# Kernel optimization log

Hardware: AMD Instinct MI355X
Metric: run time of the kernel (lower is better)

Reference implementation:

```python
import jax, jax.numpy as jnp
import numpy as np

N_EMBED = 256
HEAD_SIZE = 64
B, T = 32, 768

def setup_inputs() -> dict:
    key = jax.random.key(0)
    kx, kq, kk, kv = jax.random.split(key, 4)
    bound = 1.0 / np.sqrt(N_EMBED)  # torch nn.Linear default init
    return {
        "x": jax.random.normal(kx, (B, T, N_EMBED), dtype=jnp.float32),
        "wq": jax.random.uniform(kq, (N_EMBED, HEAD_SIZE), minval=-bound, maxval=bound, dtype=jnp.float32),
        "wk": jax.random.uniform(kk, (N_EMBED, HEAD_SIZE), minval=-bound, maxval=bound, dtype=jnp.float32),
        "wv": jax.random.uniform(kv, (N_EMBED, HEAD_SIZE), minval=-bound, maxval=bound, dtype=jnp.float32),
    }

def reference(x, wq, wk, wv):
    # x: [B, T, C]; wq/wk/wv: [C, H]
    q = jnp.einsum('btc,ch->bth', x, wq)
    k = jnp.einsum('btc,ch->bth', x, wk)
    v = jnp.einsum('btc,ch->bth', x, wv)
    scale = k.shape[-1] ** -0.5
    scores = jnp.einsum('bqh,bkh->bqk', q, k) * scale  # [B, T, T]
    Tn = x.shape[1]
    causal = jnp.tril(jnp.ones((Tn, Tn), dtype=bool))
    scores = jnp.where(causal, scores, -jnp.inf)
    attn = jax.nn.softmax(scores, axis=-1)
    # dropout omitted (eval mode) for deterministic reference
    return jnp.einsum('bqk,bkh->bqh', attn, v)
```

## Files before the change

kernel.cpp:

```cpp
#include <hip/hip_runtime.h>
#include <hip/hip_bf16.h>

#define B_  32
#define T_  768
#define C_  256
#define H_  64
#define BT_ (B_*T_)
#define WT_OFF (3*BT_*H_)

using short8 = __attribute__((ext_vector_type(8))) short;
using f32x4  = __attribute__((ext_vector_type(4))) float;

__device__ __forceinline__ ushort f2bf(float f) {
    union { float f; unsigned u; } v; v.f = f;
    unsigned u = v.u;
    return (ushort)((u + 0x7FFFu + ((u >> 16) & 1u)) >> 16);
}

__global__ __launch_bounds__(256) void prep_w_kernel(
    const float* __restrict__ wq, const float* __restrict__ wk,
    const float* __restrict__ wv, ushort* __restrict__ ws)
{
    const int idx = blockIdx.x*256 + threadIdx.x;
    const int m = idx >> 14, r = idx & 16383;
    const int h = r >> 8, k = r & 255;
    const float* w = (m == 0) ? wq : (m == 1) ? wk : wv;
    ws[WT_OFF + idx] = f2bf(w[k*H_ + h]);
}

__global__ __launch_bounds__(256) void qkv_proj_kernel(
    const float* __restrict__ x, ushort* __restrict__ ws)
{
    __shared__ ushort wT[64][264];
    __shared__ ushort vls[64][72];
    const int tid   = threadIdx.x;
    const int wv_id = tid >> 6;
    const int lane  = tid & 63;
    const int g     = lane >> 4;
    const int c     = lane & 15;
    const int rowbase = blockIdx.x*64;
    const int row     = rowbase + wv_id*16 + c;
    const int sh = tid >> 2, ss = tid & 3;

    short8 a[8];
    const float* xr = x + row*C_;
    #pragma unroll
    for (int ch = 0; ch < 8; ++ch) {
        const float4 f0 = *(const float4*)(xr + ch*32 + g*8);
        const float4 f1 = *(const float4*)(xr + ch*32 + g*8 + 4);
        short8 t;
        t[0]=(short)f2bf(f0.x); t[1]=(short)f2bf(f0.y); t[2]=(short)f2bf(f0.z); t[3]=(short)f2bf(f0.w);
        t[4]=(short)f2bf(f1.x); t[5]=(short)f2bf(f1.y); t[6]=(short)f2bf(f1.z); t[7]=(short)f2bf(f1.w);
        a[ch] = t;
    }

    const ushort* wtg = ws + WT_OFF;
    #pragma unroll
    for (int i = 0; i < 8; ++i)
        *(short8*)&wT[sh][ss*64 + i*8] = *(const short8*)(wtg + sh*256 + ss*64 + i*8);
    __syncthreads();

    for (int m = 0; m < 3; ++m) {
        #pragma unroll
        for (int jn = 0; jn < 4; ++jn) {
            f32x4 acc = {0.f, 0.f, 0.f, 0.f};
            #pragma unroll
            for (int ch = 0; ch < 8; ++ch) {
                const short8 bw = *(const short8*)(&wT[jn*16 + c][ch*32 + g*8]);
                acc = __builtin_amdgcn_mfma_f32_16x16x32_bf16(a[ch], bw, acc, 0, 0, 0);
            }
            if (m == 0) {
                #pragma unroll
                for (int r = 0; r < 4; ++r)
                    vls[wv_id*16 + g*4 + r][jn*16 + c] = f2bf(acc[r] * 0.125f);
            } else if (m == 1) {
                #pragma unroll
                for (int r = 0; r < 4; ++r)
                    vls[wv_id*16 + g*4 + r][jn*16 + c] = f2bf(acc[r]);
            } else {
                #pragma unroll
                for (int r = 0; r < 4; ++r)
                    vls[jn*16 + c][wv_id*16 + g*4 + r] = f2bf(acc[r]);
            }
        }
        __syncthreads();
        {
            ushort* dst = (m < 2)
                ? (ws + m*BT_*H_ + (rowbase + sh)*H_ + ss*16)
                : (ws + 2*BT_*H_ + sh*BT_ + rowbase + ss*16);
            *(short8*)(dst)     = *(const short8*)&vls[sh][ss*16];
            *(short8*)(dst + 8) = *(const short8*)&vls[sh][ss*16 + 8];
            if (m < 2) {
                const ushort* src = wtg + (m+1)*16384 + sh*256 + ss*64;
                #pragma unroll
                for (int i = 0; i < 8; ++i)
                    *(short8*)&wT[sh][ss*64 + i*8] = *(const short8*)(src + i*8);
            }
        }
        __syncthreads();
    }
}

__global__ __launch_bounds__(256) void attn_kernel(
    const ushort* __restrict__ ws, float* __restrict__ out)
{
    __shared__ ushort kls[2][64][72];
    __shared__ ushort vls[2][64][72];
    __shared__ ushort pls[4][16][72];

    const int tid   = threadIdx.x;
    const int wv_id = tid >> 6;
    const int lane  = tid & 63;
    const int g     = lane >> 4;
    const int c     = lane & 15;
    const int qt    = 11 - (blockIdx.x >> 5);
    const int b     = blockIdx.x & 31;
    const int nkt   = qt + 1;
    const int sh = tid >> 2, ss = tid & 3;

    const ushort* kg  = ws + BT_*H_ + b*T_*H_;
    const ushort* vtg = ws + 2*BT_*H_ + b*T_;

    short8 aq[2];
    const ushort* qp = ws + (b*T_ + qt*64 + wv_id*16 + c)*H_;
    aq[0] = *(const short8*)(qp + g*8);
    aq[1] = *(const short8*)(qp + 32 + g*8);

    float m_ = -INFINITY, l_ = 0.f;
    f32x4 o[4];
    #pragma unroll
    for (int jh = 0; jh < 4; ++jh) o[jh] = (f32x4){0.f, 0.f, 0.f, 0.f};

    short8 kreg0, kreg1, vreg0, vreg1;
    #define LOAD_TILES(kt_) do { \
        const ushort* ksrc = kg + ((kt_)*64 + sh)*H_ + ss*16;       \
        kreg0 = *(const short8*)ksrc; kreg1 = *(const short8*)(ksrc + 8); \
        const ushort* vsrc = vtg + sh*BT_ + (kt_)*64 + ss*16;       \
        vreg0 = *(const short8*)vsrc; vreg1 = *(const short8*)(vsrc + 8); \
    } while (0)
    #define WRITE_TILES(bi_) do { \
        *(short8*)&kls[bi_][sh][ss*16]     = kreg0; \
        *(short8*)&kls[bi_][sh][ss*16 + 8] = kreg1; \
        *(short8*)&vls[bi_][sh][ss*16]     = vreg0; \
        *(short8*)&vls[bi_][sh][ss*16 + 8] = vreg1; \
    } while (0)

    LOAD_TILES(0);
    WRITE_TILES(0);
    __syncthreads();

    int cur = 0;
    for (int kt = 0; kt < nkt; ++kt) {
        const bool more = (kt + 1 < nkt);
        if (more) LOAD_TILES(kt + 1);

        f32x4 s[4];
        #pragma unroll
        for (int j = 0; j < 4; ++j) {
            f32x4 acc = {0.f, 0.f, 0.f, 0.f};
            #pragma unroll
            for (int ch = 0; ch < 2; ++ch) {
                const short8 bk = *(const short8*)(&kls[cur][j*16 + c][ch*32 + g*8]);
                acc = __builtin_amdgcn_mfma_f32_16x16x32_bf16(bk, aq[ch], acc, 0, 0, 0);
            }
            s[j] = acc;
        }

        if (kt == qt) {
            const int qloc = wv_id*16 + c;
            #pragma unroll
            for (int j = 0; j < 4; ++j)
                #pragma unroll
                for (int r = 0; r < 4; ++r)
                    if (j*16 + g*4 + r > qloc) s[j][r] = -1e30f;
        }

        float tm = s[0][0];
        #pragma unroll
        for (int j = 0; j < 4; ++j)
            #pragma unroll
            for (int r = 0; r < 4; ++r) tm = fmaxf(tm, s[j][r]);
        tm = fmaxf(tm, __shfl_xor(tm, 16));
        tm = fmaxf(tm, __shfl_xor(tm, 32));
        const float mn = fmaxf(m_, tm);
        const float al = __expf(m_ - mn);
        m_ = mn;
        float ps = 0.f;
        #pragma unroll
        for (int j = 0; j < 4; ++j)
            #pragma unroll
            for (int r = 0; r < 4; ++r) {
                const float p = __expf(s[j][r] - mn);
                s[j][r] = p;
                ps += p;
            }
        ps += __shfl_xor(ps, 16);
        ps += __shfl_xor(ps, 32);
        l_ = l_*al + ps;

        #pragma unroll
        for (int r = 0; r < 4; ++r) {
            const float alr = __shfl(al, g*4 + r);
            #pragma unroll
            for (int jh = 0; jh < 4; ++jh) o[jh][r] *= alr;
        }

        #pragma unroll
        for (int j = 0; j < 4; ++j) {
            const uint lo = (uint)f2bf(s[j][0]) | ((uint)f2bf(s[j][1]) << 16);
            const uint hi = (uint)f2bf(s[j][2]) | ((uint)f2bf(s[j][3]) << 16);
            *(uint2*)&pls[wv_id][c][j*16 + g*4] = make_uint2(lo, hi);
        }

        #pragma unroll
        for (int c2 = 0; c2 < 2; ++c2) {
            const short8 ap = *(const short8*)(&pls[wv_id][c][c2*32 + g*8]);
            #pragma unroll
            for (int jh = 0; jh < 4; ++jh) {
                const short8 bv = *(const short8*)(&vls[cur][jh*16 + c][c2*32 + g*8]);
                o[jh] = __builtin_amdgcn_mfma_f32_16x16x32_bf16(ap, bv, o[jh], 0, 0, 0);
            }
        }

        if (more) WRITE_TILES(cur ^ 1);
        __syncthreads();
        cur ^= 1;
    }

    float* op = out + (b*T_ + qt*64 + wv_id*16)*H_;
    #pragma unroll
    for (int r = 0; r < 4; ++r) {
        const float lr  = __shfl(l_, g*4 + r);
        const float inv = 1.0f / lr;
        #pragma unroll
        for (int jh = 0; jh < 4; ++jh)
            op[(g*4 + r)*H_ + jh*16 + c] = o[jh][r] * inv;
    }
    #undef LOAD_TILES
    #undef WRITE_TILES
}

extern "C" void kernel_launch(void* const* d_in, const int* in_sizes, int n_in,
                              void* d_out, int out_size, void* d_ws, size_t ws_size,
                              hipStream_t stream) {
    const float* x  = (const float*)d_in[0];
    const float* wq = (const float*)d_in[1];
    const float* wk = (const float*)d_in[2];
    const float* wv = (const float*)d_in[3];
    ushort* ws = (ushort*)d_ws;

    prep_w_kernel<<<dim3(192), dim3(256), 0, stream>>>(wq, wk, wv, ws);
    qkv_proj_kernel<<<dim3(BT_/64), dim3(256), 0, stream>>>(x, ws);
    attn_kernel<<<dim3(B_*12), dim3(256), 0, stream>>>(ws, (float*)d_out);
}
```

Measured before the change: 103.8 us.

## Fuse weight prep, QKV projection and attention into one cooperative kernel

Replaces the three kernel launches (weight transpose/convert, QKV projection, attention) with a single cooperative kernel. Each block projects the 64 rows it will later attend over, keeps Q in LDS and registers instead of writing it to global memory, and stages fp32 weights directly into LDS as bf16. K and V^T are still written to the workspace and a grid-wide sync separates projection from attention. Query tiles are paired short/long per batch to balance causal work. This removes launch gaps and the Q round trip, but adds a grid barrier, redundant per-block weight conversion, and requires all 384 blocks to be co-resident.

```diff
diff --git a/kernel.cpp b/kernel.cpp
--- a/kernel.cpp
+++ b/kernel.cpp
@@ -1,12 +1,13 @@
 #include <hip/hip_runtime.h>
 #include <hip/hip_bf16.h>
+#include <hip/hip_cooperative_groups.h>
 
 #define B_  32
 #define T_  768
 #define C_  256
 #define H_  64
 #define BT_ (B_*T_)
-#define WT_OFF (3*BT_*H_)
+#define VT_OFF (BT_*H_)
 
 using short8 = __attribute__((ext_vector_type(8))) short;
 using f32x4  = __attribute__((ext_vector_type(4))) float;
@@ -17,114 +18,103 @@
     return (ushort)((u + 0x7FFFu + ((u >> 16) & 1u)) >> 16);
 }
 
-__global__ __launch_bounds__(256) void prep_w_kernel(
-    const float* __restrict__ wq, const float* __restrict__ wk,
-    const float* __restrict__ wv, ushort* __restrict__ ws)
+__device__ __forceinline__ void stage_w(const float* __restrict__ wsrc,
+                                        ushort (*wT)[264], int tid) {
+    #pragma unroll
+    for (int j = 0; j < 16; ++j) {
+        const int base = tid*4 + j*1024;
+        const float4 f = *(const float4*)(wsrc + base);
+        const int k = base >> 6, h0 = base & 63;
+        wT[h0+0][k] = f2bf(f.x); wT[h0+1][k] = f2bf(f.y);
+        wT[h0+2][k] = f2bf(f.z); wT[h0+3][k] = f2bf(f.w);
+    }
+}
+
+__global__ __launch_bounds__(256, 2) void fused_kernel(
+    const float* __restrict__ x, const float* __restrict__ wq,
+    const float* __restrict__ wk, const float* __restrict__ wv,
+    ushort* __restrict__ ws, float* __restrict__ out)
 {
-    const int idx = blockIdx.x*256 + threadIdx.x;
-    const int m = idx >> 14, r = idx & 16383;
-    const int h = r >> 8, k = r & 255;
-    const float* w = (m == 0) ? wq : (m == 1) ? wk : wv;
-    ws[WT_OFF + idx] = f2bf(w[k*H_ + h]);
-}
-
-__global__ __launch_bounds__(256) void qkv_proj_kernel(
-    const float* __restrict__ x, ushort* __restrict__ ws)
-{
-    __shared__ ushort wT[64][264];
-    __shared__ ushort vls[64][72];
+    union Smem {
+        struct { ushort wT[64][264]; ushort qls[64][72]; ushort vls[64][72]; } p;
+        struct { ushort kls[2][64][72]; ushort vls[2][64][72]; ushort pls[4][16][72]; } a;
+    };
+    __shared__ Smem sm;
+
     const int tid   = threadIdx.x;
     const int wv_id = tid >> 6;
     const int lane  = tid & 63;
     const int g     = lane >> 4;
     const int c     = lane & 15;
-    const int rowbase = blockIdx.x*64;
-    const int row     = rowbase + wv_id*16 + c;
+    const int u     = blockIdx.x >> 1;
+    const int b     = u / 6;
+    const int q6    = u - b*6;
+    const int qt    = (blockIdx.x & 1) ? (11 - q6) : q6;
+    const int rowbase = b*T_ + qt*64;
     const int sh = tid >> 2, ss = tid & 3;
 
-    short8 a[8];
-    const float* xr = x + row*C_;
-    #pragma unroll
-    for (int ch = 0; ch < 8; ++ch) {
-        const float4 f0 = *(const float4*)(xr + ch*32 + g*8);
-        const float4 f1 = *(const float4*)(xr + ch*32 + g*8 + 4);
-        short8 t;
-        t[0]=(short)f2bf(f0.x); t[1]=(short)f2bf(f0.y); t[2]=(short)f2bf(f0.z); t[3]=(short)f2bf(f0.w);
-        t[4]=(short)f2bf(f1.x); t[5]=(short)f2bf(f1.y); t[6]=(short)f2bf(f1.z); t[7]=(short)f2bf(f1.w);
-        a[ch] = t;
-    }
-
-    const ushort* wtg = ws + WT_OFF;
-    #pragma unroll
-    for (int i = 0; i < 8; ++i)
-        *(short8*)&wT[sh][ss*64 + i*8] = *(const short8*)(wtg + sh*256 + ss*64 + i*8);
-    __syncthreads();
-
-    for (int m = 0; m < 3; ++m) {
-        #pragma unroll
-        for (int jn = 0; jn < 4; ++jn) {
-            f32x4 acc = {0.f, 0.f, 0.f, 0.f};
-            #pragma unroll
-            for (int ch = 0; ch < 8; ++ch) {
-                const short8 bw = *(const short8*)(&wT[jn*16 + c][ch*32 + g*8]);
-                acc = __builtin_amdgcn_mfma_f32_16x16x32_bf16(a[ch], bw, acc, 0, 0, 0);
-            }
-            if (m == 0) {
-                #pragma unroll
-                for (int r = 0; r < 4; ++r)
-                    vls[wv_id*16 + g*4 + r][jn*16 + c] = f2bf(acc[r] * 0.125f);
-            } else if (m == 1) {
-                #pragma unroll
-                for (int r = 0; r < 4; ++r)
-                    vls[wv_id*16 + g*4 + r][jn*16 + c] = f2bf(acc[r]);
-            } else {
-                #pragma unroll
-                for (int r = 0; r < 4; ++r)
-                    vls[jn*16 + c][wv_id*16 + g*4 + r] = f2bf(acc[r]);
-            }
-        }
-        __syncthreads();
-        {
-            ushort* dst = (m < 2)
-                ? (ws + m*BT_*H_ + (rowbase + sh)*H_ + ss*16)
-                : (ws + 2*BT_*H_ + sh*BT_ + rowbase + ss*16);
-            *(short8*)(dst)     = *(const short8*)&vls[sh][ss*16];
-            *(short8*)(dst + 8) = *(const short8*)&vls[sh][ss*16 + 8];
-            if (m < 2) {
-                const ushort* src = wtg + (m+1)*16384 + sh*256 + ss*64;
-                #pragma unroll
-                for (int i = 0; i < 8; ++i)
-                    *(short8*)&wT[sh][ss*64 + i*8] = *(const short8*)(src + i*8);
-            }
-        }
-        __syncthreads();
-    }
-}
-
-__global__ __launch_bounds__(256) void attn_kernel(
-    const ushort* __restrict__ ws, float* __restrict__ out)
-{
-    __shared__ ushort kls[2][64][72];
-    __shared__ ushort vls[2][64][72];
-    __shared__ ushort pls[4][16][72];
-
-    const int tid   = threadIdx.x;
-    const int wv_id = tid >> 6;
-    const int lane  = tid & 63;
-    const int g     = lane >> 4;
-    const int c     = lane & 15;
-    const int qt    = 11 - (blockIdx.x >> 5);
-    const int b     = blockIdx.x & 31;
-    const int nkt   = qt + 1;
-    const int sh = tid >> 2, ss = tid & 3;
-
-    const ushort* kg  = ws + BT_*H_ + b*T_*H_;
-    const ushort* vtg = ws + 2*BT_*H_ + b*T_;
-
+    short8 a_[8];
+    {
+        const float* xr = x + (rowbase + wv_id*16 + c)*C_;
+        #pragma unroll
+        for (int ch = 0; ch < 8; ++ch) {
+            const float4 f0 = *(const float4*)(xr + ch*32 + g*8);
+            const float4 f1 = *(const float4*)(xr + ch*32 + g*8 + 4);
+            short8 t;
+            t[0]=(short)f2bf(f0.x); t[1]=(short)f2bf(f0.y); t[2]=(short)f2bf(f0.z); t[3]=(short)f2bf(f0.w);
+            t[4]=(short)f2bf(f1.x); t[5]=(short)f2bf(f1.y); t[6]=(short)f2bf(f1.z); t[7]=(short)f2bf(f1.w);
+            a_[ch] = t;
+        }
+    }
+
+    #define PROJ_MFMA(OUT_STMT) \
+        _Pragma("unroll") \
+        for (int jn = 0; jn < 4; ++jn) { \
+            f32x4 acc = {0.f, 0.f, 0.f, 0.f}; \
+            _Pragma("unroll") \
+            for (int ch = 0; ch < 8; ++ch) { \
+                const short8 bw = *(const short8*)(&sm.p.wT[jn*16 + c][ch*32 + g*8]); \
+                acc = __builtin_amdgcn_mfma_f32_16x16x32_bf16(a_[ch], bw, acc, 0, 0, 0); \
+            } \
+            _Pragma("unroll") \
+            for (int r = 0; r < 4; ++r) { OUT_STMT; } \
+        }
+
+    stage_w(wq, sm.p.wT, tid);
+    __syncthreads();
+    PROJ_MFMA(sm.p.qls[wv_id*16 + g*4 + r][jn*16 + c] = f2bf(acc[r] * 0.125f));
+    __syncthreads();
     short8 aq[2];
-    const ushort* qp = ws + (b*T_ + qt*64 + wv_id*16 + c)*H_;
-    aq[0] = *(const short8*)(qp + g*8);
-    aq[1] = *(const short8*)(qp + 32 + g*8);
+    aq[0] = *(const short8*)&sm.p.qls[wv_id*16 + c][g*8];
+    aq[1] = *(const short8*)&sm.p.qls[wv_id*16 + c][32 + g*8];
+    stage_w(wk, sm.p.wT, tid);
+    __syncthreads();
+
+    PROJ_MFMA(sm.p.vls[wv_id*16 + g*4 + r][jn*16 + c] = f2bf(acc[r]));
+    __syncthreads();
+    {
+        ushort* dst = ws + (rowbase + sh)*H_ + ss*16;
+        *(short8*)(dst)     = *(const short8*)&sm.p.vls[sh][ss*16];
+        *(short8*)(dst + 8) = *(const short8*)&sm.p.vls[sh][ss*16 + 8];
+    }
+    stage_w(wv, sm.p.wT, tid);
+    __syncthreads();
+
+    PROJ_MFMA(sm.p.vls[jn*16 + c][wv_id*16 + g*4 + r] = f2bf(acc[r]));
+    __syncthreads();
+    {
+        ushort* dst = ws + VT_OFF + sh*BT_ + rowbase + ss*16;
+        *(short8*)(dst)     = *(const short8*)&sm.p.vls[sh][ss*16];
+        *(short8*)(dst + 8) = *(const short8*)&sm.p.vls[sh][ss*16 + 8];
+    }
+    #undef PROJ_MFMA
+
+    __threadfence();
+    cooperative_groups::this_grid().sync();
+
+    const ushort* kg  = ws + b*T_*H_;
+    const ushort* vtg = ws + VT_OFF + b*T_;
+    const int nkt = qt + 1;
 
     float m_ = -INFINITY, l_ = 0.f;
     f32x4 o[4];
@@ -139,10 +129,10 @@
         vreg0 = *(const short8*)vsrc; vreg1 = *(const short8*)(vsrc + 8); \
     } while (0)
     #define WRITE_TILES(bi_) do { \
-        *(short8*)&kls[bi_][sh][ss*16]     = kreg0; \
-        *(short8*)&kls[bi_][sh][ss*16 + 8] = kreg1; \
-        *(short8*)&vls[bi_][sh][ss*16]     = vreg0; \
-        *(short8*)&vls[bi_][sh][ss*16 + 8] = vreg1; \
+        *(short8*)&sm.a.kls[bi_][sh][ss*16]     = kreg0; \
+        *(short8*)&sm.a.kls[bi_][sh][ss*16 + 8] = kreg1; \
+        *(short8*)&sm.a.vls[bi_][sh][ss*16]     = vreg0; \
+        *(short8*)&sm.a.vls[bi_][sh][ss*16 + 8] = vreg1; \
     } while (0)
 
     LOAD_TILES(0);
@@ -160,7 +150,7 @@
             f32x4 acc = {0.f, 0.f, 0.f, 0.f};
             #pragma unroll
             for (int ch = 0; ch < 2; ++ch) {
-                const short8 bk = *(const short8*)(&kls[cur][j*16 + c][ch*32 + g*8]);
+                const short8 bk = *(const short8*)(&sm.a.kls[cur][j*16 + c][ch*32 + g*8]);
                 acc = __builtin_amdgcn_mfma_f32_16x16x32_bf16(bk, aq[ch], acc, 0, 0, 0);
             }
             s[j] = acc;
@@ -209,15 +199,15 @@
         for (int j = 0; j < 4; ++j) {
             const uint lo = (uint)f2bf(s[j][0]) | ((uint)f2bf(s[j][1]) << 16);
             const uint hi = (uint)f2bf(s[j][2]) | ((uint)f2bf(s[j][3]) << 16);
-            *(uint2*)&pls[wv_id][c][j*16 + g*4] = make_uint2(lo, hi);
+            *(uint2*)&sm.a.pls[wv_id][c][j*16 + g*4] = make_uint2(lo, hi);
         }
 
         #pragma unroll
         for (int c2 = 0; c2 < 2; ++c2) {
-            const short8 ap = *(const short8*)(&pls[wv_id][c][c2*32 + g*8]);
+            const short8 ap = *(const short8*)(&sm.a.pls[wv_id][c][c2*32 + g*8]);
             #pragma unroll
             for (int jh = 0; jh < 4; ++jh) {
-                const short8 bv = *(const short8*)(&vls[cur][jh*16 + c][c2*32 + g*8]);
+                const short8 bv = *(const short8*)(&sm.a.vls[cur][jh*16 + c][c2*32 + g*8]);
                 o[jh] = __builtin_amdgcn_mfma_f32_16x16x32_bf16(ap, bv, o[jh], 0, 0, 0);
             }
         }
@@ -227,7 +217,7 @@
         cur ^= 1;
     }
 
-    float* op = out + (b*T_ + qt*64 + wv_id*16)*H_;
+    float* op = out + (rowbase + wv_id*16)*H_;
     #pragma unroll
     for (int r = 0; r < 4; ++r) {
         const float lr  = __shfl(l_, g*4 + r);
@@ -247,9 +237,9 @@
     const float* wq = (const float*)d_in[1];
     const float* wk = (const float*)d_in[2];
     const float* wv = (const float*)d_in[3];
-    ushort* ws = (ushort*)d_ws;
-
-    prep_w_kernel<<<dim3(192), dim3(256), 0, stream>>>(wq, wk, wv, ws);
-    qkv_proj_kernel<<<dim3(BT_/64), dim3(256), 0, stream>>>(x, ws);
-    attn_kernel<<<dim3(B_*12), dim3(256), 0, stream>>>(ws, (float*)d_out);
-}
+    ushort* ws  = (ushort*)d_ws;
+    float* outp = (float*)d_out;
+
+    void* args[] = {(void*)&x, (void*)&wq, (void*)&wk, (void*)&wv, (void*)&ws, (void*)&outp};
+    hipLaunchCooperativeKernel((void*)fused_kernel, dim3(384), dim3(256), args, 0, stream);
+}
```

New measurement: 194.6 us. 87.5% more time.

## Process two query tiles per attention block to reuse staged K/V tiles

Applied to the files above, without the earlier changes.

Each attention block now computes two adjacent 64-row query tiles, keeping separate online-softmax state and output accumulators for each. Both tiles share the same K/V tiles staged in shared memory, which halves K/V global traffic and halves the block count. The trade-off is that the grid halves to 192 blocks, so fewer CUs are busy, and each block's serial work roughly doubles, along with higher register pressure.

```diff
diff --git a/kernel.cpp b/kernel.cpp
--- a/kernel.cpp
+++ b/kernel.cpp
@@ -113,23 +113,29 @@
     const int lane  = tid & 63;
     const int g     = lane >> 4;
     const int c     = lane & 15;
-    const int qt    = 11 - (blockIdx.x >> 5);
+    const int qs    = 5 - (blockIdx.x >> 5);
     const int b     = blockIdx.x & 31;
-    const int nkt   = qt + 1;
+    const int qtA   = 2*qs, qtB = 2*qs + 1;
+    const int nkt   = qtB + 1;
     const int sh = tid >> 2, ss = tid & 3;
 
     const ushort* kg  = ws + BT_*H_ + b*T_*H_;
     const ushort* vtg = ws + 2*BT_*H_ + b*T_;
 
-    short8 aq[2];
-    const ushort* qp = ws + (b*T_ + qt*64 + wv_id*16 + c)*H_;
-    aq[0] = *(const short8*)(qp + g*8);
-    aq[1] = *(const short8*)(qp + 32 + g*8);
-
-    float m_ = -INFINITY, l_ = 0.f;
-    f32x4 o[4];
-    #pragma unroll
-    for (int jh = 0; jh < 4; ++jh) o[jh] = (f32x4){0.f, 0.f, 0.f, 0.f};
+    short8 aq[2][2];
+    #pragma unroll
+    for (int u = 0; u < 2; ++u) {
+        const ushort* qp = ws + (b*T_ + (qtA + u)*64 + wv_id*16 + c)*H_;
+        aq[u][0] = *(const short8*)(qp + g*8);
+        aq[u][1] = *(const short8*)(qp + 32 + g*8);
+    }
+
+    float m_[2] = {-INFINITY, -INFINITY}, l_[2] = {0.f, 0.f};
+    f32x4 o[2][4];
+    #pragma unroll
+    for (int u = 0; u < 2; ++u)
+        #pragma unroll
+        for (int jh = 0; jh < 4; ++jh) o[u][jh] = (f32x4){0.f, 0.f, 0.f, 0.f};
 
     short8 kreg0, kreg1, vreg0, vreg1;
     #define LOAD_TILES(kt_) do { \
@@ -154,71 +160,77 @@
         const bool more = (kt + 1 < nkt);
         if (more) LOAD_TILES(kt + 1);
 
-        f32x4 s[4];
-        #pragma unroll
-        for (int j = 0; j < 4; ++j) {
-            f32x4 acc = {0.f, 0.f, 0.f, 0.f};
-            #pragma unroll
-            for (int ch = 0; ch < 2; ++ch) {
-                const short8 bk = *(const short8*)(&kls[cur][j*16 + c][ch*32 + g*8]);
-                acc = __builtin_amdgcn_mfma_f32_16x16x32_bf16(bk, aq[ch], acc, 0, 0, 0);
-            }
-            s[j] = acc;
-        }
-
-        if (kt == qt) {
-            const int qloc = wv_id*16 + c;
+        #pragma unroll
+        for (int u = 0; u < 2; ++u) {
+            const int qtu = qtA + u;
+            if (kt > qtu) continue;
+
+            f32x4 s[4];
+            #pragma unroll
+            for (int j = 0; j < 4; ++j) {
+                f32x4 acc = {0.f, 0.f, 0.f, 0.f};
+                #pragma unroll
+                for (int ch = 0; ch < 2; ++ch) {
+                    const short8 bk = *(const short8*)(&kls[cur][j*16 + c][ch*32 + g*8]);
+                    acc = __builtin_amdgcn_mfma_f32_16x16x32_bf16(bk, aq[u][ch], acc, 0, 0, 0);
+                }
+                s[j] = acc;
+            }
+
+            if (kt == qtu) {
+                const int qloc = wv_id*16 + c;
+                #pragma unroll
+                for (int j = 0; j < 4; ++j)
+                    #pragma unroll
+                    for (int r = 0; r < 4; ++r)
+                        if (j*16 + g*4 + r > qloc) s[j][r] = -1e30f;
+            }
+
+            float tm = s[0][0];
             #pragma unroll
             for (int j = 0; j < 4; ++j)
                 #pragma unroll
-                for (int r = 0; r < 4; ++r)
-                    if (j*16 + g*4 + r > qloc) s[j][r] = -1e30f;
-        }
-
-        float tm = s[0][0];
-        #pragma unroll
-        for (int j = 0; j < 4; ++j)
-            #pragma unroll
-            for (int r = 0; r < 4; ++r) tm = fmaxf(tm, s[j][r]);
-        tm = fmaxf(tm, __shfl_xor(tm, 16));
-        tm = fmaxf(tm, __shfl_xor(tm, 32));
-        const float mn = fmaxf(m_, tm);
-        const float al = __expf(m_ - mn);
-        m_ = mn;
-        float ps = 0.f;
-        #pragma unroll
-        for (int j = 0; j < 4; ++j)
+                for (int r = 0; r < 4; ++r) tm = fmaxf(tm, s[j][r]);
+            tm = fmaxf(tm, __shfl_xor(tm, 16));
+            tm = fmaxf(tm, __shfl_xor(tm, 32));
+            const float mn = fmaxf(m_[u], tm);
+            const float al = __expf(m_[u] - mn);
+            m_[u] = mn;
+            float ps = 0.f;
+            #pragma unroll
+            for (int j = 0; j < 4; ++j)
+                #pragma unroll
+                for (int r = 0; r < 4; ++r) {
+                    const float p = __expf(s[j][r] - mn);
+                    s[j][r] = p;
+                    ps += p;
+                }
+            ps += __shfl_xor(ps, 16);
+            ps += __shfl_xor(ps, 32);
+            l_[u] = l_[u]*al + ps;
+
             #pragma unroll
             for (int r = 0; r < 4; ++r) {
-                const float p = __expf(s[j][r] - mn);
-                s[j][r] = p;
-                ps += p;
-            }
-        ps += __shfl_xor(ps, 16);
-        ps += __shfl_xor(ps, 32);
-        l_ = l_*al + ps;
-
-        #pragma unroll
-        for (int r = 0; r < 4; ++r) {
-            const float alr = __shfl(al, g*4 + r);
-            #pragma unroll
-            for (int jh = 0; jh < 4; ++jh) o[jh][r] *= alr;
-        }
-
-        #pragma unroll
-        for (int j = 0; j < 4; ++j) {
-            const uint lo = (uint)f2bf(s[j][0]) | ((uint)f2bf(s[j][1]) << 16);
-            const uint hi = (uint)f2bf(s[j][2]) | ((uint)f2bf(s[j][3]) << 16);
-            *(uint2*)&pls[wv_id][c][j*16 + g*4] = make_uint2(lo, hi);
-        }
-
-        #pragma unroll
-        for (int c2 = 0; c2 < 2; ++c2) {
-            const short8 ap = *(const short8*)(&pls[wv_id][c][c2*32 + g*8]);
-            #pragma unroll
-            for (int jh = 0; jh < 4; ++jh) {
-                const short8 bv = *(const short8*)(&vls[cur][jh*16 + c][c2*32 + g*8]);
-                o[jh] = __builtin_amdgcn_mfma_f32_16x16x32_bf16(ap, bv, o[jh], 0, 0, 0);
+                const float alr = __shfl(al, g*4 + r);
+                #pragma unroll
+                for (int jh = 0; jh < 4; ++jh) o[u][jh][r] *= alr;
+            }
+
+            #pragma unroll
+            for (int j = 0; j < 4; ++j) {
+                const uint lo = (uint)f2bf(s[j][0]) | ((uint)f2bf(s[j][1]) << 16);
+                const uint hi = (uint)f2bf(s[j][2]) | ((uint)f2bf(s[j][3]) << 16);
+                *(uint2*)&pls[wv_id][c][j*16 + g*4] = make_uint2(lo, hi);
+            }
+
+            #pragma unroll
+            for (int c2 = 0; c2 < 2; ++c2) {
+                const short8 ap = *(const short8*)(&pls[wv_id][c][c2*32 + g*8]);
+                #pragma unroll
+                for (int jh = 0; jh < 4; ++jh) {
+                    const short8 bv = *(const short8*)(&vls[cur][jh*16 + c][c2*32 + g*8]);
+                    o[u][jh] = __builtin_amdgcn_mfma_f32_16x16x32_bf16(ap, bv, o[u][jh], 0, 0, 0);
+                }
             }
         }
 
@@ -227,14 +239,17 @@
         cur ^= 1;
     }
 
-    float* op = out + (b*T_ + qt*64 + wv_id*16)*H_;
-    #pragma unroll
-    for (int r = 0; r < 4; ++r) {
-        const float lr  = __shfl(l_, g*4 + r);
-        const float inv = 1.0f / lr;
-        #pragma unroll
-        for (int jh = 0; jh < 4; ++jh)
-            op[(g*4 + r)*H_ + jh*16 + c] = o[jh][r] * inv;
+    #pragma unroll
+    for (int u = 0; u < 2; ++u) {
+        float* op = out + (b*T_ + (qtA + u)*64 + wv_id*16)*H_;
+        #pragma unroll
+        for (int r = 0; r < 4; ++r) {
+            const float lr  = __shfl(l_[u], g*4 + r);
+            const float inv = 1.0f / lr;
+            #pragma unroll
+            for (int jh = 0; jh < 4; ++jh)
+                op[(g*4 + r)*H_ + jh*16 + c] = o[u][jh][r] * inv;
+        }
     }
     #undef LOAD_TILES
     #undef WRITE_TILES
@@ -251,5 +266,5 @@
 
     prep_w_kernel<<<dim3(192), dim3(256), 0, stream>>>(wq, wk, wv, ws);
     qkv_proj_kernel<<<dim3(BT_/64), dim3(256), 0, stream>>>(x, ws);
-    attn_kernel<<<dim3(B_*12), dim3(256), 0, stream>>>(ws, (float*)d_out);
-}
+    attn_kernel<<<dim3(32*6), dim3(256), 0, stream>>>(ws, (float*)d_out);
+}
```

Result: slower. 113.6 us (+9.5%).

## Split attention into one-wave blocks reading K/V directly from global memory

Applied to the files above, without the earlier changes.

The attention kernel changes from 256-thread blocks sharing double-buffered K/V tiles in LDS to 64-thread single-wave blocks. Each wave now reads its K and V^T operands straight from global memory (through cache), with no LDS staging and no block barriers. This makes four times as many blocks, which should balance the causal workload better and remove sync overhead. The cost is four times the redundant K/V global/L2 traffic per query tile and less latency hiding, since loads are no longer prefetched.

```diff
diff --git a/kernel.cpp b/kernel.cpp
--- a/kernel.cpp
+++ b/kernel.cpp
@@ -101,22 +101,18 @@
     }
 }
 
-__global__ __launch_bounds__(256) void attn_kernel(
+__global__ __launch_bounds__(64) void attn_kernel(
     const ushort* __restrict__ ws, float* __restrict__ out)
 {
-    __shared__ ushort kls[2][64][72];
-    __shared__ ushort vls[2][64][72];
-    __shared__ ushort pls[4][16][72];
-
-    const int tid   = threadIdx.x;
-    const int wv_id = tid >> 6;
-    const int lane  = tid & 63;
+    __shared__ ushort pls[16][72];
+
+    const int lane  = threadIdx.x;
     const int g     = lane >> 4;
     const int c     = lane & 15;
-    const int qt    = 11 - (blockIdx.x >> 5);
-    const int b     = blockIdx.x & 31;
+    const int qt    = 11 - (blockIdx.x >> 7);
+    const int b     = (blockIdx.x >> 2) & 31;
+    const int wv_id = blockIdx.x & 3;
     const int nkt   = qt + 1;
-    const int sh = tid >> 2, ss = tid & 3;
 
     const ushort* kg  = ws + BT_*H_ + b*T_*H_;
     const ushort* vtg = ws + 2*BT_*H_ + b*T_;
@@ -131,36 +127,15 @@
     #pragma unroll
     for (int jh = 0; jh < 4; ++jh) o[jh] = (f32x4){0.f, 0.f, 0.f, 0.f};
 
-    short8 kreg0, kreg1, vreg0, vreg1;
-    #define LOAD_TILES(kt_) do { \
-        const ushort* ksrc = kg + ((kt_)*64 + sh)*H_ + ss*16;       \
-        kreg0 = *(const short8*)ksrc; kreg1 = *(const short8*)(ksrc + 8); \
-        const ushort* vsrc = vtg + sh*BT_ + (kt_)*64 + ss*16;       \
-        vreg0 = *(const short8*)vsrc; vreg1 = *(const short8*)(vsrc + 8); \
-    } while (0)
-    #define WRITE_TILES(bi_) do { \
-        *(short8*)&kls[bi_][sh][ss*16]     = kreg0; \
-        *(short8*)&kls[bi_][sh][ss*16 + 8] = kreg1; \
-        *(short8*)&vls[bi_][sh][ss*16]     = vreg0; \
-        *(short8*)&vls[bi_][sh][ss*16 + 8] = vreg1; \
-    } while (0)
-
-    LOAD_TILES(0);
-    WRITE_TILES(0);
-    __syncthreads();
-
-    int cur = 0;
     for (int kt = 0; kt < nkt; ++kt) {
-        const bool more = (kt + 1 < nkt);
-        if (more) LOAD_TILES(kt + 1);
-
         f32x4 s[4];
         #pragma unroll
         for (int j = 0; j < 4; ++j) {
+            const ushort* krow = kg + (kt*64 + j*16 + c)*H_;
             f32x4 acc = {0.f, 0.f, 0.f, 0.f};
             #pragma unroll
             for (int ch = 0; ch < 2; ++ch) {
-                const short8 bk = *(const short8*)(&kls[cur][j*16 + c][ch*32 + g*8]);
+                const short8 bk = *(const short8*)(krow + ch*32 + g*8);
                 acc = __builtin_amdgcn_mfma_f32_16x16x32_bf16(bk, aq[ch], acc, 0, 0, 0);
             }
             s[j] = acc;
@@ -209,22 +184,18 @@
         for (int j = 0; j < 4; ++j) {
             const uint lo = (uint)f2bf(s[j][0]) | ((uint)f2bf(s[j][1]) << 16);
             const uint hi = (uint)f2bf(s[j][2]) | ((uint)f2bf(s[j][3]) << 16);
-            *(uint2*)&pls[wv_id][c][j*16 + g*4] = make_uint2(lo, hi);
+            *(uint2*)&pls[c][j*16 + g*4] = make_uint2(lo, hi);
         }
 
         #pragma unroll
         for (int c2 = 0; c2 < 2; ++c2) {
-            const short8 ap = *(const short8*)(&pls[wv_id][c][c2*32 + g*8]);
+            const short8 ap = *(const short8*)(&pls[c][c2*32 + g*8]);
             #pragma unroll
             for (int jh = 0; jh < 4; ++jh) {
-                const short8 bv = *(const short8*)(&vls[cur][jh*16 + c][c2*32 + g*8]);
+                const short8 bv = *(const short8*)(vtg + (jh*16 + c)*BT_ + kt*64 + c2*32 + g*8);
                 o[jh] = __builtin_amdgcn_mfma_f32_16x16x32_bf16(ap, bv, o[jh], 0, 0, 0);
             }
         }
-
-        if (more) WRITE_TILES(cur ^ 1);
-        __syncthreads();
-        cur ^= 1;
     }
 
     float* op = out + (b*T_ + qt*64 + wv_id*16)*H_;
@@ -236,8 +207,6 @@
         for (int jh = 0; jh < 4; ++jh)
             op[(g*4 + r)*H_ + jh*16 + c] = o[jh][r] * inv;
     }
-    #undef LOAD_TILES
-    #undef WRITE_TILES
 }
 
 extern "C" void kernel_launch(void* const* d_in, const int* in_sizes, int n_in,
@@ -251,5 +220,5 @@
 
     prep_w_kernel<<<dim3(192), dim3(256), 0, stream>>>(wq, wk, wv, ws);
     qkv_proj_kernel<<<dim3(BT_/64), dim3(256), 0, stream>>>(x, ws);
-    attn_kernel<<<dim3(B_*12), dim3(256), 0, stream>>>(ws, (float*)d_out);
-}
+    attn_kernel<<<dim3(12*32*4), dim3(64), 0, stream>>>(ws, (float*)d_out);
+}
```

Measured after the change: 111.6 us. +7.6%, slower.
